# Optimization experiments

Hardware: AMD Instinct MI355X
Metric: run time of the kernel (lower is better)

Reference implementation:

```python
import jax, jax.numpy as jnp
import numpy as np

K = 2          # kernel_size
NQ = 4         # n_qubits = K*K
NL = 2         # n_layers


def setup_inputs() -> dict:
    key = jax.random.key(0)
    ks = jax.random.split(key, 6)
    x = jax.random.uniform(ks[0], (64, 1, 128, 128), jnp.float32, 0.0, np.pi)
    conv_w = jax.random.normal(ks[1], (1, 1, K, K), jnp.float32) * 0.5
    conv_b = jax.random.normal(ks[2], (1,), jnp.float32) * 0.1
    ry_angles = jax.random.normal(ks[3], (NL, NQ), jnp.float32)  # fixed RY params
    head_w = jax.random.normal(ks[4], (1, 2), jnp.float32) * 0.5
    head_b = jax.random.normal(ks[5], (1,), jnp.float32) * 0.1
    return {"x": x, "conv_w": conv_w, "conv_b": conv_b,
            "ry_angles": ry_angles, "head_w": head_w, "head_b": head_b}


def _rx(state, theta, wire):
    # state: (N, 2,2,2,2) complex; theta: (N,) batched angle
    ax = wire + 1
    st = jnp.moveaxis(state, ax, 1)
    s0, s1 = st[:, 0], st[:, 1]                      # (N, 2,2,2)
    c = jnp.cos(theta * 0.5).reshape((-1, 1, 1, 1))
    s = jnp.sin(theta * 0.5).reshape((-1, 1, 1, 1))
    n0 = c * s0 - 1j * s * s1
    n1 = -1j * s * s0 + c * s1
    return jnp.moveaxis(jnp.stack([n0, n1], axis=1), 1, ax)


def _ry(state, phi, wire):
    # phi: scalar shared angle
    ax = wire + 1
    st = jnp.moveaxis(state, ax, 1)
    s0, s1 = st[:, 0], st[:, 1]
    c = jnp.cos(phi * 0.5)
    s = jnp.sin(phi * 0.5)
    n0 = c * s0 - s * s1
    n1 = s * s0 + c * s1
    return jnp.moveaxis(jnp.stack([n0, n1], axis=1), 1, ax)


def _cnot(state, ctrl, tgt):
    ca, ta = ctrl + 1, tgt + 1
    st = jnp.moveaxis(state, (ca, ta), (1, 2))       # (N, 2, 2, rest)
    new = jnp.stack([st[:, 0], st[:, 1, ::-1]], axis=1)  # flip target where ctrl=1
    return jnp.moveaxis(new, (1, 2), (ca, ta))


def _quantum_expval_z0(patch_flat, ry_angles):
    # patch_flat: (N, 4) -> expval PauliZ(wire 0), shape (N,)
    N = patch_flat.shape[0]
    state = jnp.zeros((N, 2, 2, 2, 2), jnp.complex64).at[:, 0, 0, 0, 0].set(1.0)
    for w in range(NQ):
        state = _rx(state, patch_flat[:, w], w)
    for l in range(NL):
        for w in range(NQ):
            state = _ry(state, ry_angles[l, w], w)
        for w in range(0, NQ - 1, 2):
            state = _cnot(state, w, w + 1)
    p = jnp.real(state) ** 2 + jnp.imag(state) ** 2   # (N,2,2,2,2)
    return p[:, 0].sum(axis=(1, 2, 3)) - p[:, 1].sum(axis=(1, 2, 3))


def reference(x, conv_w, conv_b, ry_angles, head_w, head_b):
    B, _, H, W = x.shape
    # all KxK sliding patches, feature order (c, kh, kw) row-major == patch.view(-1)
    patches = jax.lax.conv_general_dilated_patches(x, (K, K), (1, 1), 'VALID')  # (B,4,Ph,Pw)
    Ph, Pw = patches.shape[2], patches.shape[3]
    pf = patches.transpose(0, 2, 3, 1).reshape(-1, K * K)   # (N, 4)
    conv_out = pf @ conv_w.reshape(K * K) + conv_b[0]       # (N,)
    q_out = _quantum_expval_z0(pf, ry_angles)               # (N,)
    per_patch = head_w[0, 0] * conv_out + head_w[0, 1] * q_out + head_b[0]
    out = per_patch.reshape(B, Ph * Pw).mean(axis=1)        # mean over windows
    return out[:, None]
```

## Files before the change

kernel.cpp:

```cpp
#include <hip/hip_runtime.h>
#include <math.h>


#define XH 128
#define XW 128
#define PH 127
#define PW 127
#define NP (PH * PW)
#define NB 64
#define BLK 512

__global__ __launch_bounds__(BLK) void convdual_kernel(
    const float* __restrict__ x,
    const float* __restrict__ conv_w,
    const float* __restrict__ conv_b,
    const float* __restrict__ ry,
    const float* __restrict__ head_w,
    const float* __restrict__ head_b,
    float* __restrict__ out)
{
    __shared__ float sc[5];
    __shared__ float red[BLK / 64];

    const int b   = blockIdx.x;
    const int tid = threadIdx.x;

    if (tid == 0) {
        float U[4][4];
        for (int i = 0; i < 4; ++i)
            for (int j = 0; j < 4; ++j)
                U[i][j] = (i == j) ? 1.f : 0.f;
        for (int l = 0; l < 2; ++l) {
            float c0 = cosf(0.5f * ry[l * 4 + 0]), s0 = sinf(0.5f * ry[l * 4 + 0]);
            float c1 = cosf(0.5f * ry[l * 4 + 1]), s1 = sinf(0.5f * ry[l * 4 + 1]);
            for (int q1 = 0; q1 < 2; ++q1)
                for (int c = 0; c < 4; ++c) {
                    float a = U[q1][c], d = U[2 + q1][c];
                    U[q1][c]     = c0 * a - s0 * d;
                    U[2 + q1][c] = s0 * a + c0 * d;
                }
            for (int k = 0; k < 2; ++k)
                for (int c = 0; c < 4; ++c) {
                    float a = U[2 * k][c], d = U[2 * k + 1][c];
                    U[2 * k][c]     = c1 * a - s1 * d;
                    U[2 * k + 1][c] = s1 * a + c1 * d;
                }
            for (int c = 0; c < 4; ++c) {
                float t = U[2][c]; U[2][c] = U[3][c]; U[3][c] = t;
            }
        }
        float pA = 0, pB = 0, pC = 0, pD = 0, pAD = 0, pBC = 0;
        for (int k = 0; k < 4; ++k) {
            float g = (k < 2) ? 1.f : -1.f;
            pA  += g * U[k][0] * U[k][0];
            pB  += g * U[k][1] * U[k][1];
            pC  += g * U[k][2] * U[k][2];
            pD  += g * U[k][3] * U[k][3];
            pAD += g * U[k][0] * U[k][3];
            pBC += g * U[k][1] * U[k][2];
        }
        sc[0] = 0.25f * (pA + pB + pC + pD);
        sc[1] = 0.25f * (pA + pB - pC - pD);
        sc[2] = 0.25f * (pA - pB + pC - pD);
        sc[3] = 0.25f * (pA - pB - pC + pD);
        sc[4] = 0.50f * (pBC - pAD);
    }
    __syncthreads();

    const float w0 = conv_w[0], w1 = conv_w[1], w2 = conv_w[2], w3 = conv_w[3];
    const float hw0 = head_w[0], hw1 = head_w[1];
    const float k1 = sc[1], k2 = sc[2], k3 = sc[3], k4 = sc[4];
    const float cconst = hw0 * conv_b[0] + hw1 * sc[0] + head_b[0];

    const float* __restrict__ xb = x + (size_t)b * XH * XW;

    float acc = 0.f;
    for (int p = tid; p < NP; p += BLK) {
        int i = p / PW;
        int j = p - i * PW;
        float x00 = xb[i * XW + j];
        float x01 = xb[i * XW + j + 1];
        float x10 = xb[(i + 1) * XW + j];
        float x11 = xb[(i + 1) * XW + j + 1];
        float conv = w0 * x00 + w1 * x01 + w2 * x10 + w3 * x11;
        float s0, c0, s1, c1;
        __sincosf(x00, &s0, &c0);
        __sincosf(x01, &s1, &c1);
        float q = k1 * c0 + k2 * c1 + k3 * c0 * c1 + k4 * s0 * s1;
        acc += hw0 * conv + hw1 * q;
    }

    for (int off = 32; off > 0; off >>= 1)
        acc += __shfl_down(acc, off, 64);
    int wave = tid >> 6;
    if ((tid & 63) == 0) red[wave] = acc;
    __syncthreads();
    if (tid == 0) {
        float tot = 0.f;
        for (int w = 0; w < BLK / 64; ++w) tot += red[w];
        out[b] = tot * (1.0f / NP) + cconst;
    }
}

extern "C" void kernel_launch(void* const* d_in, const int* in_sizes, int n_in,
                              void* d_out, int out_size, void* d_ws, size_t ws_size,
                              hipStream_t stream) {
    const float* x      = (const float*)d_in[0];
    const float* conv_w = (const float*)d_in[1];
    const float* conv_b = (const float*)d_in[2];
    const float* ry     = (const float*)d_in[3];
    const float* head_w = (const float*)d_in[4];
    const float* head_b = (const float*)d_in[5];
    float* out = (float*)d_out;

    convdual_kernel<<<NB, BLK, 0, stream>>>(x, conv_w, conv_b, ry, head_w, head_b, out);
}
```

Before: 77.05 us.

## Split per-image reduction across many blocks with a second finalize kernel

Each image's patch range is divided into slices, and each slice is processed by its own block, so the grid grows from one block per image to many. Per-slice partial sums go to workspace, and a small second kernel adds them and applies the constant terms. The old launch had only one block per image, far fewer blocks than the GPU has compute units; the split is meant to fill the device. The cost is an extra kernel launch, a workspace round trip, and the circuit coefficients being recomputed serially in every block.

```diff
diff --git a/kernel.cpp b/kernel.cpp
--- a/kernel.cpp
+++ b/kernel.cpp
@@ -4,78 +4,80 @@
 
 #define XH 128
 #define XW 128
-#define PH 127
 #define PW 127
-#define NP (PH * PW)
+#define NP (127 * 127)
 #define NB 64
-#define BLK 512
+#define SLICES 32
+#define PPB ((NP + SLICES - 1) / SLICES)
+#define BLK1 256
 
-__global__ __launch_bounds__(BLK) void convdual_kernel(
+__device__ __forceinline__ void circuit_coeffs(const float* __restrict__ ry,
+                                               float k[5]) {
+    float U[4][4] = {{1,0,0,0},{0,1,0,0},{0,0,1,0},{0,0,0,1}};
+    for (int l = 0; l < 2; ++l) {
+        float c0 = cosf(0.5f * ry[l*4+0]), s0 = sinf(0.5f * ry[l*4+0]);
+        float c1 = cosf(0.5f * ry[l*4+1]), s1 = sinf(0.5f * ry[l*4+1]);
+        for (int q1 = 0; q1 < 2; ++q1)
+            for (int c = 0; c < 4; ++c) {
+                float a = U[q1][c], d = U[2+q1][c];
+                U[q1][c]   = c0*a - s0*d;
+                U[2+q1][c] = s0*a + c0*d;
+            }
+        for (int m = 0; m < 2; ++m)
+            for (int c = 0; c < 4; ++c) {
+                float a = U[2*m][c], d = U[2*m+1][c];
+                U[2*m][c]   = c1*a - s1*d;
+                U[2*m+1][c] = s1*a + c1*d;
+            }
+        for (int c = 0; c < 4; ++c) { float t = U[2][c]; U[2][c] = U[3][c]; U[3][c] = t; }
+    }
+    float pA=0, pB=0, pC=0, pD=0, pAD=0, pBC=0;
+    for (int r = 0; r < 4; ++r) {
+        float g = (r < 2) ? 1.f : -1.f;
+        pA  += g * U[r][0] * U[r][0];
+        pB  += g * U[r][1] * U[r][1];
+        pC  += g * U[r][2] * U[r][2];
+        pD  += g * U[r][3] * U[r][3];
+        pAD += g * U[r][0] * U[r][3];
+        pBC += g * U[r][1] * U[r][2];
+    }
+    k[0] = 0.25f * (pA + pB + pC + pD);
+    k[1] = 0.25f * (pA + pB - pC - pD);
+    k[2] = 0.25f * (pA - pB + pC - pD);
+    k[3] = 0.25f * (pA - pB - pC + pD);
+    k[4] = 0.50f * (pBC - pAD);
+}
+
+__global__ __launch_bounds__(BLK1) void partial_kernel(
     const float* __restrict__ x,
     const float* __restrict__ conv_w,
-    const float* __restrict__ conv_b,
+    const float* __restrict__ head_w,
     const float* __restrict__ ry,
-    const float* __restrict__ head_w,
-    const float* __restrict__ head_b,
-    float* __restrict__ out)
+    float* __restrict__ ws)
 {
-    __shared__ float sc[5];
-    __shared__ float red[BLK / 64];
-
-    const int b   = blockIdx.x;
-    const int tid = threadIdx.x;
+    __shared__ float sk[5];
+    __shared__ float red[BLK1 / 64];
+    const int tid   = threadIdx.x;
+    const int slice = blockIdx.x;
+    const int img   = blockIdx.y;
 
     if (tid == 0) {
-        float U[4][4];
-        for (int i = 0; i < 4; ++i)
-            for (int j = 0; j < 4; ++j)
-                U[i][j] = (i == j) ? 1.f : 0.f;
-        for (int l = 0; l < 2; ++l) {
-            float c0 = cosf(0.5f * ry[l * 4 + 0]), s0 = sinf(0.5f * ry[l * 4 + 0]);
-            float c1 = cosf(0.5f * ry[l * 4 + 1]), s1 = sinf(0.5f * ry[l * 4 + 1]);
-            for (int q1 = 0; q1 < 2; ++q1)
-                for (int c = 0; c < 4; ++c) {
-                    float a = U[q1][c], d = U[2 + q1][c];
-                    U[q1][c]     = c0 * a - s0 * d;
-                    U[2 + q1][c] = s0 * a + c0 * d;
-                }
-            for (int k = 0; k < 2; ++k)
-                for (int c = 0; c < 4; ++c) {
-                    float a = U[2 * k][c], d = U[2 * k + 1][c];
-                    U[2 * k][c]     = c1 * a - s1 * d;
-                    U[2 * k + 1][c] = s1 * a + c1 * d;
-                }
-            for (int c = 0; c < 4; ++c) {
-                float t = U[2][c]; U[2][c] = U[3][c]; U[3][c] = t;
-            }
-        }
-        float pA = 0, pB = 0, pC = 0, pD = 0, pAD = 0, pBC = 0;
-        for (int k = 0; k < 4; ++k) {
-            float g = (k < 2) ? 1.f : -1.f;
-            pA  += g * U[k][0] * U[k][0];
-            pB  += g * U[k][1] * U[k][1];
-            pC  += g * U[k][2] * U[k][2];
-            pD  += g * U[k][3] * U[k][3];
-            pAD += g * U[k][0] * U[k][3];
-            pBC += g * U[k][1] * U[k][2];
-        }
-        sc[0] = 0.25f * (pA + pB + pC + pD);
-        sc[1] = 0.25f * (pA + pB - pC - pD);
-        sc[2] = 0.25f * (pA - pB + pC - pD);
-        sc[3] = 0.25f * (pA - pB - pC + pD);
-        sc[4] = 0.50f * (pBC - pAD);
+        float k[5];
+        circuit_coeffs(ry, k);
+        for (int i = 0; i < 5; ++i) sk[i] = k[i];
     }
     __syncthreads();
 
     const float w0 = conv_w[0], w1 = conv_w[1], w2 = conv_w[2], w3 = conv_w[3];
     const float hw0 = head_w[0], hw1 = head_w[1];
-    const float k1 = sc[1], k2 = sc[2], k3 = sc[3], k4 = sc[4];
-    const float cconst = hw0 * conv_b[0] + hw1 * sc[0] + head_b[0];
+    const float k1 = sk[1], k2 = sk[2], k3 = sk[3], k4 = sk[4];
 
-    const float* __restrict__ xb = x + (size_t)b * XH * XW;
+    const float* __restrict__ xb = x + (size_t)img * XH * XW;
+    const int p0 = slice * PPB;
+    const int p1 = (p0 + PPB < NP) ? p0 + PPB : NP;
 
     float acc = 0.f;
-    for (int p = tid; p < NP; p += BLK) {
+    for (int p = p0 + tid; p < p1; p += BLK1) {
         int i = p / PW;
         int j = p - i * PW;
         float x00 = xb[i * XW + j];
@@ -86,20 +88,35 @@
         float s0, c0, s1, c1;
         __sincosf(x00, &s0, &c0);
         __sincosf(x01, &s1, &c1);
-        float q = k1 * c0 + k2 * c1 + k3 * c0 * c1 + k4 * s0 * s1;
-        acc += hw0 * conv + hw1 * q;
+        acc += hw0 * conv + hw1 * (k1 * c0 + k2 * c1 + k3 * c0 * c1 + k4 * s0 * s1);
     }
 
     for (int off = 32; off > 0; off >>= 1)
         acc += __shfl_down(acc, off, 64);
-    int wave = tid >> 6;
-    if ((tid & 63) == 0) red[wave] = acc;
+    if ((tid & 63) == 0) red[tid >> 6] = acc;
     __syncthreads();
     if (tid == 0) {
-        float tot = 0.f;
-        for (int w = 0; w < BLK / 64; ++w) tot += red[w];
-        out[b] = tot * (1.0f / NP) + cconst;
+        float t = 0.f;
+        for (int w = 0; w < BLK1 / 64; ++w) t += red[w];
+        ws[img * SLICES + slice] = t;
     }
+}
+
+__global__ __launch_bounds__(64) void final_kernel(
+    const float* __restrict__ ws,
+    const float* __restrict__ conv_b,
+    const float* __restrict__ ry,
+    const float* __restrict__ head_w,
+    const float* __restrict__ head_b,
+    float* __restrict__ out)
+{
+    const int b = threadIdx.x;
+    float k[5];
+    circuit_coeffs(ry, k);
+    float sum = 0.f;
+    for (int s = 0; s < SLICES; ++s) sum += ws[b * SLICES + s];
+    const float cconst = head_w[0] * conv_b[0] + head_w[1] * k[0] + head_b[0];
+    out[b] = sum * (1.0f / NP) + cconst;
 }
 
 extern "C" void kernel_launch(void* const* d_in, const int* in_sizes, int n_in,
@@ -112,6 +129,9 @@
     const float* head_w = (const float*)d_in[4];
     const float* head_b = (const float*)d_in[5];
     float* out = (float*)d_out;
+    float* ws  = (float*)d_ws;
 
-    convdual_kernel<<<NB, BLK, 0, stream>>>(x, conv_w, conv_b, ry, head_w, head_b, out);
+    dim3 grid1(SLICES, NB);
+    partial_kernel<<<grid1, BLK1, 0, stream>>>(x, conv_w, head_w, ry, ws);
+    final_kernel<<<1, 64, 0, stream>>>(ws, conv_b, ry, head_w, head_b, out);
 }
```

After: 69.79 us. 9.4% less time.
